# Kernel optimization log

Hardware: AMD Instinct MI355X
Metric: run time of the kernel (lower is better)

The kernel has to match this reference:

```python
import math
import jax, jax.numpy as jnp
import numpy as np

B, T, C = 4, 2048, 1024
N_HEAD = 16
HEAD_DIM = C // N_HEAD


def setup_inputs() -> dict:
    key = jax.random.key(0)
    k1, k2, k3 = jax.random.split(key, 3)
    x = jax.random.normal(k1, (B, T, C), dtype=jnp.float32)
    # nn.Linear weights: (out_features, in_features); init scale ~1/sqrt(C)
    w_attn = jax.random.normal(k2, (3 * C, C), dtype=jnp.float32) / math.sqrt(C)
    w_proj = jax.random.normal(k3, (C, C), dtype=jnp.float32) / math.sqrt(C)
    return {"x": x, "w_attn": w_attn, "w_proj": w_proj}


def reference(x, w_attn, w_proj):
    Bx, Tx, Cx = x.shape
    qkv = x @ w_attn.T  # (B,T,3C)
    q, k, v = jnp.split(qkv, 3, axis=2)
    # (B,T,H,D) -> (B,H,T,D)
    q = q.reshape(Bx, Tx, N_HEAD, HEAD_DIM).transpose(0, 2, 1, 3)
    k = k.reshape(Bx, Tx, N_HEAD, HEAD_DIM).transpose(0, 2, 1, 3)
    v = v.reshape(Bx, Tx, N_HEAD, HEAD_DIM).transpose(0, 2, 1, 3)
    scale = 1.0 / math.sqrt(HEAD_DIM)
    att = jnp.einsum("bhqd,bhkd->bhqk", q, k) * scale
    causal = jnp.tril(jnp.ones((Tx, Tx), dtype=bool))
    att = jnp.where(causal[None, None, :, :], att, -jnp.inf)
    att = jax.nn.softmax(att, axis=-1)
    out = jnp.einsum("bhqk,bhkd->bhqd", att, v)
    out = out.transpose(0, 2, 1, 3).reshape(Bx, Tx, Cx)
    return out @ w_proj.T
```

## Files before the change

### kernel.cpp

```cpp
#include <hip/hip_runtime.h>
#include <hip/hip_bf16.h>


typedef __attribute__((ext_vector_type(8))) short bf16x8;
typedef __attribute__((ext_vector_type(4))) float f32x4;
typedef __attribute__((ext_vector_type(16))) float f32x16;
typedef unsigned short ushort_t;

#if __has_builtin(__builtin_amdgcn_exp2f)
#define EXP2(x) __builtin_amdgcn_exp2f(x)
#else
#define EXP2(x) exp2f(x)
#endif

__device__ inline ushort_t f2bf(float f) {
    union { float f; unsigned int u; } x; x.f = f;
    return (ushort_t)((x.u + 0x7fffu + ((x.u >> 16) & 1u)) >> 16);
}

__device__ inline ushort_t f2bf_fast(float f) {
    union { float f; unsigned int u; } x; x.f = f;
    return (ushort_t)((x.u + 0x8000u) >> 16);
}

__device__ inline bf16x8 load8_f32_to_bf16(const float* p) {
    float4 f0 = *(const float4*)p;
    float4 f1 = *(const float4*)(p + 4);
    bf16x8 r;
    r[0] = (short)f2bf(f0.x); r[1] = (short)f2bf(f0.y);
    r[2] = (short)f2bf(f0.z); r[3] = (short)f2bf(f0.w);
    r[4] = (short)f2bf(f1.x); r[5] = (short)f2bf(f1.y);
    r[6] = (short)f2bf(f1.z); r[7] = (short)f2bf(f1.w);
    return r;
}

__device__ inline void gl2lds16(const ushort_t* g, ushort_t* l) {
    __builtin_amdgcn_global_load_lds(
        (const __attribute__((address_space(1))) unsigned int*)g,
        (__attribute__((address_space(3))) unsigned int*)l,
        16, 0, 0);
}

__global__ void cvt3(const float* __restrict__ a, long n8a,
                     const float* __restrict__ b, long n8b,
                     const float* __restrict__ c, long n8c,
                     ushort_t* __restrict__ out) {
    long i = (long)blockIdx.x * 256 + threadIdx.x;
    const float* src; long off;
    if (i < n8a) { src = a; off = i; }
    else if (i < n8a + n8b) { src = b; off = i - n8a; }
    else if (i < n8a + n8b + n8c) { src = c; off = i - n8a - n8b; }
    else return;
    *(bf16x8*)(out + i * 8) = load8_f32_to_bf16(src + off * 8);
}

__global__ void fill_zero_f32(float* out, int n) {
    int i = blockIdx.x * 256 + threadIdx.x;
    if (i < n) out[i] = 0.0f;
}

#define BM 128
#define BN 128
#define BK 64

#define QK_LOG2E_SCALE 0.18033688011112042f

template <int EPI>
__global__ __launch_bounds__(256) void gemm_lds(
        const ushort_t* __restrict__ A, const ushort_t* __restrict__ B,
        void* __restrict__ Cp, void* __restrict__ Cp2,
        int M, int N, int K) {
    __shared__ ushort_t As[BM * BK];
    __shared__ ushort_t Bs[BN * BK];

    const int tid  = threadIdx.x;
    const int lane = tid & 63;
    const int w    = tid >> 6;
    const int l31  = lane & 31;
    const int half = lane >> 5;

    const int bm = blockIdx.y * BM;
    const int bn = blockIdx.x * BN;
    const int wm = (w & 1) * 64;
    const int wn = (w >> 1) * 64;

    const int lr8 = lane >> 3;
    const int cbg = ((lane & 7) ^ lr8) * 8;
    const ushort_t* Aw = A + (size_t)(bm + w * 32 + lr8) * K + cbg;
    const ushort_t* Bw = B + (size_t)(bn + w * 32 + lr8) * K + cbg;
    ushort_t* Asw = &As[(w * 32) * BK];
    ushort_t* Bsw = &Bs[(w * 32) * BK];

    f32x16 acc[2][2] = {};

    for (int k0 = 0; k0 < K; k0 += BK) {
        if (k0) __syncthreads();
#pragma unroll
        for (int j = 0; j < 4; j++) {
            gl2lds16(Aw + (size_t)(j * 8) * K + k0, Asw + j * 8 * BK);
            gl2lds16(Bw + (size_t)(j * 8) * K + k0, Bsw + j * 8 * BK);
        }
        __syncthreads();

#pragma unroll
        for (int s = 0; s < 4; s++) {
            const int cs = (((2 * s + half) ^ (lane & 7)) * 8);
            bf16x8 af[2], bfr[2];
#pragma unroll
            for (int i = 0; i < 2; i++)
                af[i] = *(const bf16x8*)&As[(wm + i * 32 + l31) * BK + cs];
#pragma unroll
            for (int i = 0; i < 2; i++)
                bfr[i] = *(const bf16x8*)&Bs[(wn + i * 32 + l31) * BK + cs];
#pragma unroll
            for (int mi = 0; mi < 2; mi++)
#pragma unroll
                for (int ni = 0; ni < 2; ni++)
                    acc[mi][ni] = __builtin_amdgcn_mfma_f32_32x32x16_bf16(
                        af[mi], bfr[ni], acc[mi][ni], 0, 0, 0);
        }
    }

#pragma unroll
    for (int mi = 0; mi < 2; mi++)
#pragma unroll
        for (int ni = 0; ni < 2; ni++) {
            const int colg = bn + wn + ni * 32 + l31;
            if constexpr (EPI == 1) {
                float* cb = (float*)Cp + colg;
#pragma unroll
                for (int r = 0; r < 16; r++) {
                    const int row = bm + wm + mi * 32 + (r & 3) + 8 * (r >> 2) + 4 * half;
                    cb[(size_t)row * N] = acc[mi][ni][r];
                }
            } else {
                if (colg < 2048) {
                    const float qs = (colg < 1024) ? QK_LOG2E_SCALE : 1.0f;
                    ushort_t* cb = (ushort_t*)Cp + colg;
#pragma unroll
                    for (int r = 0; r < 16; r++) {
                        const int row = bm + wm + mi * 32 + (r & 3) + 8 * (r >> 2) + 4 * half;
                        cb[(size_t)row * 2048] = f2bf(acc[mi][ni][r] * qs);
                    }
                } else {
                    const int vc = colg - 2048;
                    const int hh = vc >> 6, dd = vc & 63;
                    ushort_t* vtp = (ushort_t*)Cp2 + ((size_t)hh * 64 + dd) * 2048;
#pragma unroll
                    for (int r = 0; r < 16; r++) {
                        const int row = bm + wm + mi * 32 + (r & 3) + 8 * (r >> 2) + 4 * half;
                        const int bb = row >> 11, tt = row & 2047;
                        vtp[(size_t)bb * 16 * 64 * 2048 + tt] = f2bf(acc[mi][ni][r]);
                    }
                }
            }
        }
}

#define LDK 72

template <bool A_F32, bool B_F32, int EPI>
__global__ __launch_bounds__(256) void gemm_nt(
        const void* __restrict__ Ap, const void* __restrict__ Bp,
        void* __restrict__ Cp, void* __restrict__ Cp2,
        int M, int N, int K) {
    __shared__ ushort_t As[BM * LDK];
    __shared__ ushort_t Bs[BN * LDK];

    const int tid  = threadIdx.x;
    const int lane = tid & 63;
    const int w    = tid >> 6;
    const int quad = lane >> 4;
    const int l16  = lane & 15;

    const int bm = blockIdx.y * BM;
    const int bn = blockIdx.x * BN;
    const int wm = (w & 1) * 64;
    const int wn = (w >> 1) * 64;

    f32x4 acc[4][4] = {};

    const int lrow = tid >> 3;
    const int lcol = (tid & 7) * 8;

    bf16x8 pa[4], pb[4];
#pragma unroll
    for (int i = 0; i < 4; i++) {
        const int ra = lrow + i * 32;
        if constexpr (A_F32)
            pa[i] = load8_f32_to_bf16((const float*)Ap + (size_t)(bm + ra) * K + lcol);
        else
            pa[i] = *(const bf16x8*)((const ushort_t*)Ap + (size_t)(bm + ra) * K + lcol);
        if constexpr (B_F32)
            pb[i] = load8_f32_to_bf16((const float*)Bp + (size_t)(bn + ra) * K + lcol);
        else
            pb[i] = *(const bf16x8*)((const ushort_t*)Bp + (size_t)(bn + ra) * K + lcol);
    }

    for (int k0 = 0; k0 < K; k0 += BK) {
        __syncthreads();
#pragma unroll
        for (int i = 0; i < 4; i++) {
            *(bf16x8*)&As[(lrow + i * 32) * LDK + lcol] = pa[i];
            *(bf16x8*)&Bs[(lrow + i * 32) * LDK + lcol] = pb[i];
        }
        __syncthreads();

        if (k0 + BK < K) {
            const int kn = k0 + BK + lcol;
#pragma unroll
            for (int i = 0; i < 4; i++) {
                const int ra = lrow + i * 32;
                if constexpr (A_F32)
                    pa[i] = load8_f32_to_bf16((const float*)Ap + (size_t)(bm + ra) * K + kn);
                else
                    pa[i] = *(const bf16x8*)((const ushort_t*)Ap + (size_t)(bm + ra) * K + kn);
                if constexpr (B_F32)
                    pb[i] = load8_f32_to_bf16((const float*)Bp + (size_t)(bn + ra) * K + kn);
                else
                    pb[i] = *(const bf16x8*)((const ushort_t*)Bp + (size_t)(bn + ra) * K + kn);
            }
        }

#pragma unroll
        for (int ks = 0; ks < BK; ks += 32) {
            bf16x8 af[4], bfr[4];
#pragma unroll
            for (int i = 0; i < 4; i++)
                af[i] = *(const bf16x8*)&As[(wm + i * 16 + l16) * LDK + ks + quad * 8];
#pragma unroll
            for (int i = 0; i < 4; i++)
                bfr[i] = *(const bf16x8*)&Bs[(wn + i * 16 + l16) * LDK + ks + quad * 8];
#pragma unroll
            for (int mi = 0; mi < 4; mi++)
#pragma unroll
                for (int ni = 0; ni < 4; ni++)
                    acc[mi][ni] = __builtin_amdgcn_mfma_f32_16x16x32_bf16(
                        af[mi], bfr[ni], acc[mi][ni], 0, 0, 0);
        }
    }

#pragma unroll
    for (int mi = 0; mi < 4; mi++) {
        const int row0 = bm + wm + mi * 16 + quad * 4;
#pragma unroll
        for (int r = 0; r < 4; r++) {
            const int row = row0 + r;
            if constexpr (EPI == 1) {
                float* crow = (float*)Cp + (size_t)row * N + bn + wn;
#pragma unroll
                for (int ni = 0; ni < 4; ni++)
                    crow[ni * 16 + l16] = acc[mi][ni][r];
            } else {
                if (bn < 2048) {
                    const float qs = (bn < 1024) ? QK_LOG2E_SCALE : 1.0f;
                    ushort_t* crow = (ushort_t*)Cp + (size_t)row * 2048 + bn + wn;
#pragma unroll
                    for (int ni = 0; ni < 4; ni++)
                        crow[ni * 16 + l16] = f2bf(acc[mi][ni][r] * qs);
                } else {
                    ushort_t* vt = (ushort_t*)Cp2;
                    const int bb = row >> 11, tt = row & 2047;
#pragma unroll
                    for (int ni = 0; ni < 4; ni++) {
                        const int vc = bn + wn + ni * 16 + l16 - 2048;
                        const int hh = vc >> 6, dd = vc & 63;
                        vt[(((size_t)bb * 16 + hh) * 64 + dd) * 2048 + tt] =
                            f2bf(acc[mi][ni][r]);
                    }
                }
            }
        }
    }
}

#define AT_T 2048
#define PLD 72

__global__ __launch_bounds__(256) void attn4(
        const ushort_t* __restrict__ qk,
        const ushort_t* __restrict__ vt,
        ushort_t* __restrict__ attout) {
    const int bh   = blockIdx.x;
    const int qblk = (gridDim.y - 1) - blockIdx.y;
    const int b    = bh >> 4;
    const int h    = bh & 15;

    const int tid  = threadIdx.x;
    const int lane = tid & 63;
    const int w    = tid >> 6;
    const int quad = lane >> 4;
    const int l16  = lane & 15;
    const int sw   = l16 & 7;

    __shared__ ushort_t Ks[64 * 64];
    __shared__ ushort_t Vs[80 * 64];
    __shared__ ushort_t Ps[4][32 * PLD];

    for (int i = tid; i < 16 * 64; i += 256) Vs[64 * 64 + i] = 0;
    if (tid < 64) Vs[64 * 64 + tid] = 0x3F80;

    const ushort_t* qp = qk + (size_t)b * AT_T * 2048 + h * 64;
    const ushort_t* kp = qp + 1024;
    const ushort_t* vp = vt + (size_t)bh * 64 * 2048;

    const int Q0 = qblk * 128 + w * 16;

    bf16x8 aq[2][2];
#pragma unroll
    for (int s = 0; s < 2; s++) {
        const ushort_t* qrow = qp + (size_t)(Q0 + s * 64 + l16) * 2048;
        aq[s][0] = *(const bf16x8*)(qrow + quad * 8);
        aq[s][1] = *(const bf16x8*)(qrow + 32 + quad * 8);
    }

    f32x4 o[2][5] = {};

    const int lr8 = lane >> 3;
    const int cbg = ((lane & 7) ^ lr8) * 8;

    const int nk = 2 * qblk + 2;
    for (int kt = 0; kt < nk; kt++) {
        const int k0 = kt * 64;
        if (kt) __syncthreads();
#pragma unroll
        for (int j = 0; j < 2; j++) {
            gl2lds16(kp + (size_t)(k0 + w * 16 + j * 8 + lr8) * 2048 + cbg,
                     &Ks[(w * 16 + j * 8) * 64]);
            gl2lds16(vp + (size_t)(w * 16 + j * 8 + lr8) * 2048 + k0 + cbg,
                     &Vs[(w * 16 + j * 8) * 64]);
        }
        __syncthreads();

        f32x4 s0[4], s1[4];
#pragma unroll
        for (int c = 0; c < 4; c++) {
            s0[c][0] = -8.0f; s0[c][1] = -8.0f; s0[c][2] = -8.0f; s0[c][3] = -8.0f;
            s1[c] = s0[c];
#pragma unroll
            for (int ks = 0; ks < 2; ks++) {
                const int cs = ((quad + 4 * ks) ^ sw) * 8;
                bf16x8 bk = *(const bf16x8*)&Ks[(c * 16 + l16) * 64 + cs];
                s0[c] = __builtin_amdgcn_mfma_f32_16x16x32_bf16(aq[0][ks], bk, s0[c], 0, 0, 0);
                s1[c] = __builtin_amdgcn_mfma_f32_16x16x32_bf16(aq[1][ks], bk, s1[c], 0, 0, 0);
            }
        }

        if (kt >= 2 * qblk) {
            const int q0r = Q0 + quad * 4;
#pragma unroll
            for (int c = 0; c < 4; c++) {
                const int kcol = k0 + c * 16 + l16;
#pragma unroll
                for (int r = 0; r < 4; r++)
                    if (kcol > q0r + r) s0[c][r] = -__builtin_inff();
            }
        }
        if (kt == 2 * qblk + 1) {
            const int q1r = Q0 + 64 + quad * 4;
#pragma unroll
            for (int c = 0; c < 4; c++) {
                const int kcol = k0 + c * 16 + l16;
#pragma unroll
                for (int r = 0; r < 4; r++)
                    if (kcol > q1r + r) s1[c][r] = -__builtin_inff();
            }
        }

#pragma unroll
        for (int c = 0; c < 4; c++)
#pragma unroll
            for (int r = 0; r < 4; r++) {
                Ps[w][(quad * 4 + r) * PLD + c * 16 + l16] = f2bf_fast(EXP2(s0[c][r]));
                Ps[w][(16 + quad * 4 + r) * PLD + c * 16 + l16] = f2bf_fast(EXP2(s1[c][r]));
            }

        __asm__ __volatile__("s_waitcnt lgkmcnt(0)" ::: "memory");

#pragma unroll
        for (int ks = 0; ks < 2; ks++) {
            const int cs = ((quad + 4 * ks) ^ sw) * 8;
            bf16x8 ap0 = *(const bf16x8*)&Ps[w][l16 * PLD + ks * 32 + quad * 8];
            bf16x8 ap1 = *(const bf16x8*)&Ps[w][(16 + l16) * PLD + ks * 32 + quad * 8];
#pragma unroll
            for (int n = 0; n < 5; n++) {
                bf16x8 bv = *(const bf16x8*)&Vs[(n * 16 + l16) * 64 + cs];
                o[0][n] = __builtin_amdgcn_mfma_f32_16x16x32_bf16(ap0, bv, o[0][n], 0, 0, 0);
                o[1][n] = __builtin_amdgcn_mfma_f32_16x16x32_bf16(ap1, bv, o[1][n], 0, 0, 0);
            }
        }
    }

#pragma unroll
    for (int s = 0; s < 2; s++) {
        ushort_t* op = attout + (size_t)(b * AT_T + Q0 + s * 64 + quad * 4) * 1024 + h * 64;
#pragma unroll
        for (int r = 0; r < 4; r++) {
            const float l = __shfl(o[s][4][r], lane & 48, 64);
            const float inv = 1.0f / fmaxf(l, 1e-30f);
            ushort_t* orow = op + (size_t)r * 1024;
#pragma unroll
            for (int n = 0; n < 4; n++)
                orow[n * 16 + l16] = f2bf(o[s][n][r] * inv);
        }
    }
}

extern "C" void kernel_launch(void* const* d_in, const int* in_sizes, int n_in,
                              void* d_out, int out_size, void* d_ws, size_t ws_size,
                              hipStream_t stream) {
    const float* x      = (const float*)d_in[0];
    const float* w_attn = (const float*)d_in[1];
    const float* w_proj = (const float*)d_in[2];
    float* out = (float*)d_out;

    const int M = 8192, C = 1024;
    const size_t E_QK  = (size_t)M * 2048;
    const size_t E_VT  = (size_t)4 * 16 * 64 * 2048;
    const size_t E_ATT = (size_t)M * 1024;
    const size_t E_X   = (size_t)M * 1024;
    const size_t E_WA  = (size_t)3072 * 1024;
    const size_t E_WP  = (size_t)1024 * 1024;
    const size_t need_mid  = (E_QK + E_VT + E_ATT) * 2;
    const size_t need_full = need_mid + (E_X + E_WA + E_WP) * 2;

    if (ws_size < need_mid) {
        fill_zero_f32<<<(out_size + 255) / 256, 256, 0, stream>>>(out, out_size);
        return;
    }

    ushort_t* qk  = (ushort_t*)d_ws;
    ushort_t* vt  = qk + E_QK;
    ushort_t* att = vt + E_VT;

    if (ws_size >= need_full) {
        ushort_t* xb  = att + E_ATT;
        const long n8x = (long)(E_X / 8), n8a = (long)(E_WA / 8), n8p = (long)(E_WP / 8);
        const long n8  = n8x + n8a + n8p;
        cvt3<<<(int)((n8 + 255) / 256), 256, 0, stream>>>(
            x, n8x, w_attn, n8a, w_proj, n8p, xb);

        ushort_t* wab = xb + E_X;
        ushort_t* wpb = wab + E_WA;
        gemm_lds<2><<<dim3(3 * C / BN, M / BM), 256, 0, stream>>>(
            xb, wab, qk, vt, M, 3 * C, C);
        attn4<<<dim3(64, 16), 256, 0, stream>>>(qk, vt, att);
        gemm_lds<1><<<dim3(C / BN, M / BM), 256, 0, stream>>>(
            att, wpb, out, nullptr, M, C, C);
    } else {
        gemm_nt<true, true, 2><<<dim3(3 * C / BN, M / BM), 256, 0, stream>>>(
            x, w_attn, qk, vt, M, 3 * C, C);
        attn4<<<dim3(64, 16), 256, 0, stream>>>(qk, vt, att);
        gemm_nt<false, true, 1><<<dim3(C / BN, M / BM), 256, 0, stream>>>(
            att, w_proj, out, nullptr, M, C, C);
    }
}
```

Measured before the change: 231.2 us.

## Double-buffer GEMM LDS tiles and rotate P-tile columns to avoid bank conflicts

The projection GEMM now keeps two LDS buffers for A and B and issues the global-to-LDS loads for the next K tile before computing on the current one, so memory latency can overlap with MFMA work and one barrier per iteration goes away. Separately, the attention kernel's P-tile store and load use a row-dependent column rotation to spread LDS bank accesses. The cost is double the GEMM shared memory, which can lower occupancy, and the rotation must stay consistent between the writer and reader lanes.

```diff
diff --git a/kernel.cpp b/kernel.cpp
--- a/kernel.cpp
+++ b/kernel.cpp
@@ -70,8 +70,8 @@
         const ushort_t* __restrict__ A, const ushort_t* __restrict__ B,
         void* __restrict__ Cp, void* __restrict__ Cp2,
         int M, int N, int K) {
-    __shared__ ushort_t As[BM * BK];
-    __shared__ ushort_t Bs[BN * BK];
+    __shared__ ushort_t As[2][BM * BK];
+    __shared__ ushort_t Bs[2][BN * BK];
 
     const int tid  = threadIdx.x;
     const int lane = tid & 63;
@@ -88,19 +88,23 @@
     const int cbg = ((lane & 7) ^ lr8) * 8;
     const ushort_t* Aw = A + (size_t)(bm + w * 32 + lr8) * K + cbg;
     const ushort_t* Bw = B + (size_t)(bn + w * 32 + lr8) * K + cbg;
-    ushort_t* Asw = &As[(w * 32) * BK];
-    ushort_t* Bsw = &Bs[(w * 32) * BK];
+
+    auto issue = [&](int buf, int k0) {
+#pragma unroll
+        for (int j = 0; j < 4; j++) {
+            gl2lds16(Aw + (size_t)(j * 8) * K + k0, &As[buf][(w * 32 + j * 8) * BK]);
+            gl2lds16(Bw + (size_t)(j * 8) * K + k0, &Bs[buf][(w * 32 + j * 8) * BK]);
+        }
+    };
 
     f32x16 acc[2][2] = {};
 
-    for (int k0 = 0; k0 < K; k0 += BK) {
-        if (k0) __syncthreads();
-#pragma unroll
-        for (int j = 0; j < 4; j++) {
-            gl2lds16(Aw + (size_t)(j * 8) * K + k0, Asw + j * 8 * BK);
-            gl2lds16(Bw + (size_t)(j * 8) * K + k0, Bsw + j * 8 * BK);
-        }
+    issue(0, 0);
+    const int nIt = K / BK;
+    for (int k = 0; k < nIt; k++) {
+        const int cur = k & 1;
         __syncthreads();
+        if (k + 1 < nIt) issue(cur ^ 1, (k + 1) * BK);
 
 #pragma unroll
         for (int s = 0; s < 4; s++) {
@@ -108,10 +112,10 @@
             bf16x8 af[2], bfr[2];
 #pragma unroll
             for (int i = 0; i < 2; i++)
-                af[i] = *(const bf16x8*)&As[(wm + i * 32 + l31) * BK + cs];
+                af[i] = *(const bf16x8*)&As[cur][(wm + i * 32 + l31) * BK + cs];
 #pragma unroll
             for (int i = 0; i < 2; i++)
-                bfr[i] = *(const bf16x8*)&Bs[(wn + i * 32 + l31) * BK + cs];
+                bfr[i] = *(const bf16x8*)&Bs[cur][(wn + i * 32 + l31) * BK + cs];
 #pragma unroll
             for (int mi = 0; mi < 2; mi++)
 #pragma unroll
@@ -368,20 +372,23 @@
         }
 
 #pragma unroll
-        for (int c = 0; c < 4; c++)
+        for (int c = 0; c < 4; c++) {
+            const int colr = (c * 16 + l16 + quad * 16) & 63;
 #pragma unroll
             for (int r = 0; r < 4; r++) {
-                Ps[w][(quad * 4 + r) * PLD + c * 16 + l16] = f2bf_fast(EXP2(s0[c][r]));
-                Ps[w][(16 + quad * 4 + r) * PLD + c * 16 + l16] = f2bf_fast(EXP2(s1[c][r]));
-            }
+                Ps[w][(quad * 4 + r) * PLD + colr] = f2bf_fast(EXP2(s0[c][r]));
+                Ps[w][(16 + quad * 4 + r) * PLD + colr] = f2bf_fast(EXP2(s1[c][r]));
+            }
+        }
 
         __asm__ __volatile__("s_waitcnt lgkmcnt(0)" ::: "memory");
 
 #pragma unroll
         for (int ks = 0; ks < 2; ks++) {
-            const int cs = ((quad + 4 * ks) ^ sw) * 8;
-            bf16x8 ap0 = *(const bf16x8*)&Ps[w][l16 * PLD + ks * 32 + quad * 8];
-            bf16x8 ap1 = *(const bf16x8*)&Ps[w][(16 + l16) * PLD + ks * 32 + quad * 8];
+            const int cs  = ((quad + 4 * ks) ^ sw) * 8;
+            const int pst = (ks * 32 + quad * 8 + (l16 >> 2) * 16) & 63;
+            bf16x8 ap0 = *(const bf16x8*)&Ps[w][l16 * PLD + pst];
+            bf16x8 ap1 = *(const bf16x8*)&Ps[w][(16 + l16) * PLD + pst];
 #pragma unroll
             for (int n = 0; n < 5; n++) {
                 bf16x8 bv = *(const bf16x8*)&Vs[(n * 16 + l16) * 64 + cs];
```

After: 243.5 us. 5.3% more time.

## Use wider 128x256 tile GEMM for QKV projection and swizzle P stores

Applied to the files above, without the earlier changes.

Adds a gemm_wide kernel with 128x256 output tiles (each wave computes 64x128) for the QKV projection, raising reuse of A tiles and halving the number of blocks. The old square-tile GEMM is renamed and kept for the output projection. The attention kernel also rotates the column layout of the P staging buffer per quad to reduce LDS bank conflicts on writes and reads. The wider tile needs more accumulator registers and more LDS, which may lower occupancy despite launch_bounds(256,2).

```diff
diff --git a/kernel.cpp b/kernel.cpp
--- a/kernel.cpp
+++ b/kernel.cpp
@@ -59,14 +59,110 @@
     if (i < n) out[i] = 0.0f;
 }
 
+#define BK 64
+#define QK_LOG2E_SCALE 0.18033688011112042f
+
+#define WBM 128
+#define WBN 256
+
+template <int EPI>
+__global__ __launch_bounds__(256, 2) void gemm_wide(
+        const ushort_t* __restrict__ A, const ushort_t* __restrict__ B,
+        void* __restrict__ Cp, void* __restrict__ Cp2,
+        int M, int N, int K) {
+    __shared__ ushort_t As[WBM * BK];
+    __shared__ ushort_t Bs[WBN * BK];
+
+    const int tid  = threadIdx.x;
+    const int lane = tid & 63;
+    const int w    = tid >> 6;
+    const int quad = lane >> 4;
+    const int l16  = lane & 15;
+    const int sw   = l16 & 7;
+
+    const int bm = blockIdx.y * WBM;
+    const int bn = blockIdx.x * WBN;
+    const int wm = (w & 1) * 64;
+    const int wn = (w >> 1) * 128;
+
+    const int lr8 = lane >> 3;
+    const int cbg = ((lane & 7) ^ lr8) * 8;
+    const ushort_t* Aw = A + (size_t)(bm + w * 32 + lr8) * K + cbg;
+    const ushort_t* Bw = B + (size_t)(bn + w * 64 + lr8) * K + cbg;
+    ushort_t* Asw = &As[(w * 32) * BK];
+    ushort_t* Bsw = &Bs[(w * 64) * BK];
+
+    f32x4 acc[4][8] = {};
+
+    for (int k0 = 0; k0 < K; k0 += BK) {
+        if (k0) __syncthreads();
+#pragma unroll
+        for (int j = 0; j < 4; j++)
+            gl2lds16(Aw + (size_t)(j * 8) * K + k0, Asw + j * 8 * BK);
+#pragma unroll
+        for (int j = 0; j < 8; j++)
+            gl2lds16(Bw + (size_t)(j * 8) * K + k0, Bsw + j * 8 * BK);
+        __syncthreads();
+
+#pragma unroll
+        for (int ks = 0; ks < 2; ks++) {
+            const int cs = ((quad + 4 * ks) ^ sw) * 8;
+            bf16x8 af[4], bfr[8];
+#pragma unroll
+            for (int i = 0; i < 4; i++)
+                af[i] = *(const bf16x8*)&As[(wm + i * 16 + l16) * BK + cs];
+#pragma unroll
+            for (int i = 0; i < 8; i++)
+                bfr[i] = *(const bf16x8*)&Bs[(wn + i * 16 + l16) * BK + cs];
+#pragma unroll
+            for (int mi = 0; mi < 4; mi++)
+#pragma unroll
+                for (int ni = 0; ni < 8; ni++)
+                    acc[mi][ni] = __builtin_amdgcn_mfma_f32_16x16x32_bf16(
+                        af[mi], bfr[ni], acc[mi][ni], 0, 0, 0);
+        }
+    }
+
+#pragma unroll
+    for (int mi = 0; mi < 4; mi++) {
+        const int row0 = bm + wm + mi * 16 + quad * 4;
+#pragma unroll
+        for (int r = 0; r < 4; r++) {
+            const int row = row0 + r;
+            if constexpr (EPI == 1) {
+                float* crow = (float*)Cp + (size_t)row * N + bn + wn;
+#pragma unroll
+                for (int ni = 0; ni < 8; ni++)
+                    crow[ni * 16 + l16] = acc[mi][ni][r];
+            } else {
+                const int cb0 = bn + wn;
+                if (cb0 < 2048) {
+                    const float qs = (cb0 < 1024) ? QK_LOG2E_SCALE : 1.0f;
+                    ushort_t* crow = (ushort_t*)Cp + (size_t)row * 2048 + cb0;
+#pragma unroll
+                    for (int ni = 0; ni < 8; ni++)
+                        crow[ni * 16 + l16] = f2bf(acc[mi][ni][r] * qs);
+                } else {
+                    ushort_t* vt = (ushort_t*)Cp2;
+                    const int bb = row >> 11, tt = row & 2047;
+#pragma unroll
+                    for (int ni = 0; ni < 8; ni++) {
+                        const int vc = cb0 + ni * 16 + l16 - 2048;
+                        const int hh = vc >> 6, dd = vc & 63;
+                        vt[(((size_t)bb * 16 + hh) * 64 + dd) * 2048 + tt] =
+                            f2bf(acc[mi][ni][r]);
+                    }
+                }
+            }
+        }
+    }
+}
+
 #define BM 128
 #define BN 128
-#define BK 64
-
-#define QK_LOG2E_SCALE 0.18033688011112042f
 
 template <int EPI>
-__global__ __launch_bounds__(256) void gemm_lds(
+__global__ __launch_bounds__(256) void gemm_sq(
         const ushort_t* __restrict__ A, const ushort_t* __restrict__ B,
         void* __restrict__ Cp, void* __restrict__ Cp2,
         int M, int N, int K) {
@@ -368,20 +464,23 @@
         }
 
 #pragma unroll
-        for (int c = 0; c < 4; c++)
+        for (int c = 0; c < 4; c++) {
+            const int colr = (c * 16 + l16 + quad * 16) & 63;
 #pragma unroll
             for (int r = 0; r < 4; r++) {
-                Ps[w][(quad * 4 + r) * PLD + c * 16 + l16] = f2bf_fast(EXP2(s0[c][r]));
-                Ps[w][(16 + quad * 4 + r) * PLD + c * 16 + l16] = f2bf_fast(EXP2(s1[c][r]));
-            }
+                Ps[w][(quad * 4 + r) * PLD + colr] = f2bf_fast(EXP2(s0[c][r]));
+                Ps[w][(16 + quad * 4 + r) * PLD + colr] = f2bf_fast(EXP2(s1[c][r]));
+            }
+        }
 
         __asm__ __volatile__("s_waitcnt lgkmcnt(0)" ::: "memory");
 
 #pragma unroll
         for (int ks = 0; ks < 2; ks++) {
-            const int cs = ((quad + 4 * ks) ^ sw) * 8;
-            bf16x8 ap0 = *(const bf16x8*)&Ps[w][l16 * PLD + ks * 32 + quad * 8];
-            bf16x8 ap1 = *(const bf16x8*)&Ps[w][(16 + l16) * PLD + ks * 32 + quad * 8];
+            const int cs  = ((quad + 4 * ks) ^ sw) * 8;
+            const int pst = (ks * 32 + quad * 8 + (l16 >> 2) * 16) & 63;
+            bf16x8 ap0 = *(const bf16x8*)&Ps[w][l16 * PLD + pst];
+            bf16x8 ap1 = *(const bf16x8*)&Ps[w][(16 + l16) * PLD + pst];
 #pragma unroll
             for (int n = 0; n < 5; n++) {
                 bf16x8 bv = *(const bf16x8*)&Vs[(n * 16 + l16) * 64 + cs];
@@ -442,10 +541,10 @@
 
         ushort_t* wab = xb + E_X;
         ushort_t* wpb = wab + E_WA;
-        gemm_lds<2><<<dim3(3 * C / BN, M / BM), 256, 0, stream>>>(
+        gemm_wide<2><<<dim3(3 * C / WBN, M / WBM), 256, 0, stream>>>(
             xb, wab, qk, vt, M, 3 * C, C);
         attn4<<<dim3(64, 16), 256, 0, stream>>>(qk, vt, att);
-        gemm_lds<1><<<dim3(C / BN, M / BM), 256, 0, stream>>>(
+        gemm_sq<1><<<dim3(C / BN, M / BM), 256, 0, stream>>>(
             att, wpb, out, nullptr, M, C, C);
     } else {
         gemm_nt<true, true, 2><<<dim3(3 * C / BN, M / BM), 256, 0, stream>>>(
```

New measurement: 267.9 us. 1.16x slower.
